# Optimization experiments

Measured on AMD Instinct MI355X. Metric: run time of the kernel, lower is better.

## Reference

```python
import jax, jax.numpy as jnp
import numpy as np
from jax import lax

V = 5          # IMU nodes
C = 128        # channels
T = 128        # timesteps
B = 128        # batch
K = 3          # st_kernel_size (non-causal)
V_TH = 0.8     # LIF threshold
TAU = 2.0      # LIF default tau (spikingjelly)
EPS = 1e-5


def setup_inputs() -> dict:
    key = jax.random.key(0)
    ks = jax.random.split(key, 6)
    # binary spike input [T, B, C, 2V]
    x_spike = (jax.random.uniform(ks[0], (T, B, C, 2 * V)) < 0.5).astype(jnp.float32)
    # modality fusion conv1d: [C, 2C, 1], kaiming-ish scale
    W_fusion = jax.random.normal(ks[1], (C, 2 * C, 1), jnp.float32) * (1.0 / np.sqrt(2 * C))
    gn1_w = jnp.ones((C,), jnp.float32)
    gn1_b = jnp.zeros((C,), jnp.float32)
    # node mixer conv1d over time: [V, V, K]
    W_mixer = jax.random.normal(ks[2], (V, V, K), jnp.float32) * (1.0 / np.sqrt(V * K))
    gn2_w = jnp.ones((V,), jnp.float32)
    gn2_b = jnp.zeros((V,), jnp.float32)
    # learnable adjacency: eye + 0.01*randn
    adj = jnp.eye(V, dtype=jnp.float32) + 0.01 * jax.random.normal(ks[3], (V, V), jnp.float32)
    return {"x_spike": x_spike, "W_fusion": W_fusion, "gn1_w": gn1_w, "gn1_b": gn1_b,
            "W_mixer": W_mixer, "gn2_w": gn2_w, "gn2_b": gn2_b, "adj": adj}


def groupnorm1(x, w, b):
    # single-group GroupNorm on [N, C, L]: normalize over (C, L) per sample
    mu = jnp.mean(x, axis=(1, 2), keepdims=True)
    var = jnp.var(x, axis=(1, 2), keepdims=True)
    xn = (x - mu) * lax.rsqrt(var + EPS)
    return xn * w[None, :, None] + b[None, :, None]


def lif_multistep(x_seq):
    # spikingjelly LIFNode, step_mode='m', decay_input=True, hard reset to 0
    def step(v, x):
        v = v + (x - v) / TAU
        s = (v >= V_TH).astype(x.dtype)
        v = v * (1.0 - s)
        return v, s
    _, spikes = lax.scan(step, jnp.zeros_like(x_seq[0]), x_seq)
    return spikes


def reference(x_spike, W_fusion, gn1_w, gn1_b, W_mixer, gn2_w, gn2_b, adj):
    Tn, Bn, Cn, N = x_spike.shape
    # ---- dual-modality fusion ----
    acc, gyr = x_spike[..., :V], x_spike[..., V:]
    fused = jnp.concatenate([acc, gyr], axis=2).reshape(Tn * Bn, 2 * Cn, V)  # [TB, 2C, V]
    y = jnp.einsum('oc,ncv->nov', W_fusion[:, :, 0], fused)                   # 1x1 conv
    y = groupnorm1(y, gn1_w, gn1_b)
    x_nodes = lif_multistep(y.reshape(Tn, Bn, Cn, V))                         # [T,B,C,V]
    # ---- adaptive topology temporal conv ----
    x_bt = x_nodes.transpose(1, 2, 3, 0).reshape(Bn * Cn, V, Tn)              # [BC, V, T]
    pad = K // 2
    x_bt = jnp.pad(x_bt, ((0, 0), (0, 0), (pad, pad)))
    sym = 0.5 * (adj + adj.T)
    masked_w = W_mixer * jax.nn.sigmoid(sym)[:, :, None]                      # [V, V, K]
    y_bt = lax.conv_general_dilated(x_bt, masked_w, (1,), 'VALID',
                                    dimension_numbers=('NCH', 'OIH', 'NCH'))
    y_bt = y_bt[..., :Tn]
    y_bt = groupnorm1(y_bt, gn2_w, gn2_b)
    y_mixed = y_bt.reshape(Bn, Cn, V, Tn).transpose(3, 0, 1, 2)               # [T,B,C,V]
    out = lif_multistep(y_mixed)
    return jnp.concatenate([out, out], axis=-1)                               # [T,B,C,2V]
```

## Files before the change

### kernel.cpp

```cpp
#include <hip/hip_runtime.h>
#include <cstdint>
#include <cstddef>

#define NV 5
#define NC 128
#define NT 128
#define NB 128
typedef unsigned long long ull;
typedef float f32x2 __attribute__((ext_vector_type(2)));
typedef float f32x4 __attribute__((ext_vector_type(4)));

__device__ __forceinline__ float fa(float a, float b){ return __fadd_rn(a,b); }
__device__ __forceinline__ float fm(float a, float b){ return __fmul_rn(a,b); }
__device__ __forceinline__ float fs(float a, float b){ return __fsub_rn(a,b); }

__device__ __forceinline__ f32x2 pkadd(f32x2 a, f32x2 b){
    f32x2 d; asm("v_pk_add_f32 %0, %1, %2" : "=v"(d) : "v"(a), "v"(b)); return d;
}
__device__ __forceinline__ f32x2 pkmul_lo(f32x2 a, f32x2 w){
    f32x2 d; asm("v_pk_mul_f32 %0, %1, %2 op_sel:[0,0] op_sel_hi:[1,0]"
                 : "=v"(d) : "v"(a), "v"(w)); return d;
}
__device__ __forceinline__ f32x2 pkmul_hi(f32x2 a, f32x2 w){
    f32x2 d; asm("v_pk_mul_f32 %0, %1, %2 op_sel:[0,1] op_sel_hi:[1,1]"
                 : "=v"(d) : "v"(a), "v"(w)); return d;
}

__device__ __forceinline__ float base80(const float* a)
{
    float r0=a[0],r1=a[1],r2=a[2],r3=a[3],r4=a[4],r5=a[5],r6=a[6],r7=a[7];
    #pragma unroll
    for (int i = 8; i < 80; i += 8) {
        r0=fa(r0,a[i+0]); r1=fa(r1,a[i+1]); r2=fa(r2,a[i+2]); r3=fa(r3,a[i+3]);
        r4=fa(r4,a[i+4]); r5=fa(r5,a[i+5]); r6=fa(r6,a[i+6]); r7=fa(r7,a[i+7]);
    }
    return fa(fa(fa(r0,r1),fa(r2,r3)), fa(fa(r4,r5),fa(r6,r7)));
}

__device__ __forceinline__ float base80v(const float* a, float mu)
{
    float r[8];
    #pragma unroll
    for (int j = 0; j < 8; ++j) { const float d = fs(a[j], mu); r[j] = fm(d, d); }
    #pragma unroll
    for (int i = 8; i < 80; i += 8)
        #pragma unroll
        for (int j = 0; j < 8; ++j) {
            const float d = fs(a[i + j], mu);
            r[j] = fa(r[j], fm(d, d));
        }
    return fa(fa(fa(r[0],r[1]),fa(r[2],r[3])), fa(fa(r[4],r[5]),fa(r[6],r[7])));
}

__global__ __launch_bounds__(256) void kT(const float* __restrict__ W,
                                          f32x4* __restrict__ Wt4)
{
    const int i = blockIdx.x * 256 + threadIdx.x;
    const int fcp = i >> 6, oL = i & 63;
    f32x4 p;
    p.x = W[oL * 256 + 2 * fcp];
    p.y = W[(oL + 64) * 256 + 2 * fcp];
    p.z = W[oL * 256 + 2 * fcp + 1];
    p.w = W[(oL + 64) * 256 + 2 * fcp + 1];
    Wt4[i] = p;
}

__global__ __launch_bounds__(256) void kA(const float* __restrict__ x,
                                          const f32x4* __restrict__ Wt4,
                                          const float* __restrict__ g1w,
                                          const float* __restrict__ g1b,
                                          float* __restrict__ y1)
{
    const int n0   = blockIdx.x * 8;
    const int tid  = threadIdx.x;
    const int lane = tid & 63;
    const int wv   = tid >> 6;

    __shared__ __align__(16) float xs[10240];

    {
        const float4* g0 = (const float4*)(x + (size_t)(n0 + 2 * wv) * 1280);
        const float4* g1 = g0 + 320;
        #pragma unroll
        for (int it = 0; it < 5; ++it) {
            const int k = it * 64 + lane;
            const float4 a = g0[k];
            const float4 b = g1[k];
            const float av[4] = {a.x, a.y, a.z, a.w};
            const float bv[4] = {b.x, b.y, b.z, b.w};
            int f = k * 4;
            #pragma unroll
            for (int e = 0; e < 4; ++e, ++f) {
                const int c  = f / 10;
                const int j  = f - c * 10;
                const int v  = (j < 5) ? j : j - 5;
                const int fc = (j < 5) ? c : c + 128;
                const int fcp = fc >> 1, sub = fc & 1;
                f32x2 pr; pr.x = av[e]; pr.y = bv[e];
                *(f32x2*)&xs[(fcp * 4 + wv) * 20 + sub * 10 + v * 2] = pr;
            }
        }
    }

    f32x2 accA[NV], accB[NV];
    #pragma unroll
    for (int v = 0; v < NV; ++v) { accA[v] = (f32x2){0.f,0.f}; accB[v] = (f32x2){0.f,0.f}; }

    const float* xw = xs + wv * 20;
    #pragma unroll 2
    for (int fcp = 0; fcp < 128; ++fcp) {
        const f32x4 wab = Wt4[fcp * 64 + lane];
        const float* row = xw + fcp * 80;
        const f32x4 Q0 = *(const f32x4*)&row[0];
        const f32x4 Q1 = *(const f32x4*)&row[4];
        const f32x4 Q2 = *(const f32x4*)&row[8];
        const f32x4 Q3 = *(const f32x4*)&row[12];
        const f32x4 Q4 = *(const f32x4*)&row[16];
        const f32x2 w01 = __builtin_shufflevector(wab, wab, 0, 1);
        const f32x2 w23 = __builtin_shufflevector(wab, wab, 2, 3);
        const f32x2 a0 = __builtin_shufflevector(Q0, Q0, 0, 1);
        const f32x2 a1 = __builtin_shufflevector(Q0, Q0, 2, 3);
        const f32x2 a2 = __builtin_shufflevector(Q1, Q1, 0, 1);
        const f32x2 a3 = __builtin_shufflevector(Q1, Q1, 2, 3);
        const f32x2 a4 = __builtin_shufflevector(Q2, Q2, 0, 1);
        const f32x2 b0 = __builtin_shufflevector(Q2, Q2, 2, 3);
        const f32x2 b1 = __builtin_shufflevector(Q3, Q3, 0, 1);
        const f32x2 b2 = __builtin_shufflevector(Q3, Q3, 2, 3);
        const f32x2 b3 = __builtin_shufflevector(Q4, Q4, 0, 1);
        const f32x2 b4 = __builtin_shufflevector(Q4, Q4, 2, 3);
        accA[0] = pkadd(accA[0], pkmul_lo(a0, w01));
        accA[1] = pkadd(accA[1], pkmul_lo(a1, w01));
        accA[2] = pkadd(accA[2], pkmul_lo(a2, w01));
        accA[3] = pkadd(accA[3], pkmul_lo(a3, w01));
        accA[4] = pkadd(accA[4], pkmul_lo(a4, w01));
        accB[0] = pkadd(accB[0], pkmul_hi(a0, w01));
        accB[1] = pkadd(accB[1], pkmul_hi(a1, w01));
        accB[2] = pkadd(accB[2], pkmul_hi(a2, w01));
        accB[3] = pkadd(accB[3], pkmul_hi(a3, w01));
        accB[4] = pkadd(accB[4], pkmul_hi(a4, w01));
        accA[0] = pkadd(accA[0], pkmul_lo(b0, w23));
        accA[1] = pkadd(accA[1], pkmul_lo(b1, w23));
        accA[2] = pkadd(accA[2], pkmul_lo(b2, w23));
        accA[3] = pkadd(accA[3], pkmul_lo(b3, w23));
        accA[4] = pkadd(accA[4], pkmul_lo(b4, w23));
        accB[0] = pkadd(accB[0], pkmul_hi(b0, w23));
        accB[1] = pkadd(accB[1], pkmul_hi(b1, w23));
        accB[2] = pkadd(accB[2], pkmul_hi(b2, w23));
        accB[3] = pkadd(accB[3], pkmul_hi(b3, w23));
        accB[4] = pkadd(accB[4], pkmul_hi(b4, w23));
    }
    __syncthreads();

    float* ys     = xs;
    float* statAf = xs + 5120;
    float* muS    = xs + 5152;
    float* rstdS  = xs + 5160;

    #pragma unroll
    for (int sl = 0; sl < 2; ++sl) {
        const int g = wv * 2 + sl;
        #pragma unroll
        for (int v = 0; v < NV; ++v) {
            ys[g * 640 + lane * 5 + v]        = sl ? accA[v].y : accA[v].x;
            ys[g * 640 + (lane + 64) * 5 + v] = sl ? accB[v].y : accB[v].x;
        }
    }
    __syncthreads();

    if (tid < 32) {
        const int g = tid >> 2, p = tid & 3;
        const float b0 = base80(&ys[g * 640 + (2 * p) * 80]);
        const float b1 = base80(&ys[g * 640 + (2 * p + 1) * 80]);
        statAf[g * 4 + p] = fa(b0, b1);
    }
    __syncthreads();
    if (tid < 8) {
        const int g = tid;
        const float* s = statAf + g * 4;
        const float tot = fa(fa(s[0], s[1]), fa(s[2], s[3]));
        muS[g] = __fdiv_rn(tot, 640.f);
    }
    __syncthreads();

    #pragma unroll
    for (int sl = 0; sl < 2; ++sl) {
        const int g = wv * 2 + sl;
        const float mu = muS[g];
        #pragma unroll
        for (int v = 0; v < NV; ++v) {
            const float aA = sl ? accA[v].y : accA[v].x;
            const float aB = sl ? accB[v].y : accB[v].x;
            const float dA = fs(aA, mu);
            const float dB = fs(aB, mu);
            ys[g * 640 + lane * 5 + v]        = fm(dA, dA);
            ys[g * 640 + (lane + 64) * 5 + v] = fm(dB, dB);
        }
    }
    __syncthreads();
    if (tid < 32) {
        const int g = tid >> 2, p = tid & 3;
        const float b0 = base80(&ys[g * 640 + (2 * p) * 80]);
        const float b1 = base80(&ys[g * 640 + (2 * p + 1) * 80]);
        statAf[g * 4 + p] = fa(b0, b1);
    }
    __syncthreads();
    if (tid < 8) {
        const int g = tid;
        const float* s = statAf + g * 4;
        const float tot = fa(fa(s[0], s[1]), fa(s[2], s[3]));
        const float var = __fdiv_rn(tot, 640.f);
        rstdS[g] = __fdiv_rn(1.f, __fsqrt_rn(fa(var, 1e-5f)));
    }
    __syncthreads();

    #pragma unroll
    for (int ch = 0; ch < 2; ++ch) {
        const int o = lane + ch * 64;
        const float wf = g1w[o], bf = g1b[o];
        #pragma unroll
        for (int sl = 0; sl < 2; ++sl) {
            const int g = wv * 2 + sl;
            const float mu = muS[g], rstd = rstdS[g];
            const int n = n0 + g;
            #pragma unroll
            for (int v = 0; v < NV; ++v) {
                const float av = ch ? (sl ? accB[v].y : accB[v].x)
                                    : (sl ? accA[v].y : accA[v].x);
                const float xn = fm(fs(av, mu), rstd);
                y1[(size_t)n * 640 + o * 5 + v] = fa(fm(xn, wf), bf);
            }
        }
    }
}

__global__ __launch_bounds__(320) void kB1(const float* __restrict__ y1,
                                           ulonglong2* __restrict__ masks)
{
    const int b   = blockIdx.x >> 1;
    const int c0  = (blockIdx.x & 1) * 64;
    const int tid = threadIdx.x;

    ull lo = 0ull, hi = 0ull;
    float vm = 0.f;
    const float* p = y1 + (size_t)b * 640 + (size_t)c0 * 5 + tid;
    for (int t0 = 0; t0 < NT; t0 += 16) {
        float xv[16];
        #pragma unroll
        for (int j = 0; j < 16; ++j)
            xv[j] = p[(size_t)(t0 + j) * (NB * 640)];
        #pragma unroll
        for (int j = 0; j < 16; ++j) {
            vm = fa(vm, fm(fs(xv[j], vm), 0.5f));
            if (vm >= 0.8f) {
                const int t = t0 + j;
                if (t < 64) lo |= 1ull << t; else hi |= 1ull << (t - 64);
                vm = 0.f;
            }
        }
    }
    masks[(size_t)b * 640 + (size_t)c0 * 5 + tid] = make_ulonglong2(lo, hi);
}

__device__ __forceinline__ float bitf(ull lo, ull hi, int t)
{
    if (t < 0 || t > 127) return 0.f;
    return (float)(((t < 64) ? (lo >> t) : (hi >> (t - 64))) & 1ull);
}

__global__ __launch_bounds__(512) void kB2(const ulonglong2* __restrict__ masks,
                                           const float* __restrict__ Wm,
                                           const float* __restrict__ g2w,
                                           const float* __restrict__ g2b,
                                           const float* __restrict__ adj,
                                           float* __restrict__ out)
{
    const int blk = blockIdx.x;
    const int b   = blk >> 5;
    const int c0  = (blk & 31) * 4;
    const int tid = threadIdx.x;
    const int p   = tid >> 7;
    const int lt  = tid & 127;

    __shared__ float mw_s[75];
    __shared__ ull   m_lo[4][5], m_hi[4][5];
    __shared__ float conv_s[4][5][128];
    __shared__ float spk_s[128][40];
    __shared__ float stat_s[4][8];
    __shared__ float mu_s[4], rstd_s[4];

    if (tid < 75) {
        const int oo = tid / 15, rem = tid % 15, ii = rem / 3;
        const float sym = fm(0.5f, fa(adj[oo * 5 + ii], adj[ii * 5 + oo]));
        const float e = (float)exp(-(double)sym);
        const float sig = __fdiv_rn(1.f, fa(1.f, e));
        mw_s[tid] = fm(Wm[tid], sig);
    }
    if (tid < 20) {
        const int pp = tid / 5, vv = tid % 5;
        const ulonglong2 m = masks[((size_t)b * 128 + c0 + pp) * 5 + vv];
        m_lo[pp][vv] = m.x; m_hi[pp][vv] = m.y;
    }
    __syncthreads();

    {
        float bv[5][3];
        #pragma unroll
        for (int i = 0; i < 5; ++i) {
            const ull lo = m_lo[p][i], hi = m_hi[p][i];
            #pragma unroll
            for (int k = 0; k < 3; ++k)
                bv[i][k] = bitf(lo, hi, lt - 1 + k);
        }
        #pragma unroll
        for (int o = 0; o < 5; ++o) {
            float res = 0.f;
            #pragma unroll
            for (int i = 0; i < 5; ++i)
                #pragma unroll
                for (int k = 0; k < 3; ++k)
                    res = fa(res, fm(mw_s[(o * 5 + i) * 3 + k], bv[i][k]));
            conv_s[p][o][lt] = res;
        }
    }
    __syncthreads();

    if (lt < 8)
        stat_s[p][lt] = base80(&conv_s[p][0][0] + lt * 80);
    __syncthreads();
    if (lt == 0) {
        const float* s = stat_s[p];
        const float tot = fa(fa(fa(s[0],s[1]),fa(s[2],s[3])),
                             fa(fa(s[4],s[5]),fa(s[6],s[7])));
        mu_s[p] = __fdiv_rn(tot, 640.f);
    }
    __syncthreads();

    if (lt < 8)
        stat_s[p][lt] = base80v(&conv_s[p][0][0] + lt * 80, mu_s[p]);
    __syncthreads();
    if (lt == 0) {
        const float* s = stat_s[p];
        const float tot = fa(fa(fa(s[0],s[1]),fa(s[2],s[3])),
                             fa(fa(s[4],s[5]),fa(s[6],s[7])));
        const float var = __fdiv_rn(tot, 640.f);
        rstd_s[p] = __fdiv_rn(1.f, __fsqrt_rn(fa(var, 1e-5f)));
    }
    __syncthreads();

    if (lt < 5) {
        const int o = lt;
        const float mu = mu_s[p], rstd = rstd_s[p];
        const float gw = g2w[o], gb = g2b[o];
        float vm = 0.f;
        for (int t = 0; t < NT; ++t) {
            const float z  = conv_s[p][o][t];
            const float xn = fm(fs(z, mu), rstd);
            const float yn = fa(fm(xn, gw), gb);
            vm = fa(vm, fm(fs(yn, vm), 0.5f));
            const bool sp = (vm >= 0.8f);
            if (sp) vm = 0.f;
            const float so = sp ? 1.f : 0.f;
            spk_s[t][p * 10 + o]     = so;
            spk_s[t][p * 10 + 5 + o] = so;
        }
    }
    __syncthreads();

    for (int q = tid; q < 1280; q += 512) {
        const int t = q / 10, s = q - t * 10;
        float4* dst = (float4*)(out + ((size_t)(t * NB + b) * 1280 + c0 * 10));
        dst[s] = reinterpret_cast<const float4*>(&spk_s[t][0])[s];
    }
}

extern "C" void kernel_launch(void* const* d_in, const int* in_sizes, int n_in,
                              void* d_out, int out_size, void* d_ws, size_t ws_size,
                              hipStream_t stream)
{
    const float* x   = (const float*)d_in[0];
    const float* W   = (const float*)d_in[1];
    const float* g1w = (const float*)d_in[2];
    const float* g1b = (const float*)d_in[3];
    const float* Wm  = (const float*)d_in[4];
    const float* g2w = (const float*)d_in[5];
    const float* g2b = (const float*)d_in[6];
    const float* adj = (const float*)d_in[7];
    float* out = (float*)d_out;

    float* y1 = (float*)d_ws;
    ulonglong2* masks = (ulonglong2*)((char*)d_ws + (64u << 20));
    f32x4* Wt4 = (f32x4*)((char*)d_ws + (80u << 20));

    hipLaunchKernelGGL(kT, dim3(32), dim3(256), 0, stream, W, Wt4);
    hipLaunchKernelGGL(kA, dim3(NT * NB / 8), dim3(256), 0, stream,
                       x, Wt4, g1w, g1b, y1);
    hipLaunchKernelGGL(kB1, dim3(NB * 2), dim3(320), 0, stream,
                       y1, masks);
    hipLaunchKernelGGL(kB2, dim3(4096), dim3(512), 0, stream,
                       masks, Wm, g2w, g2b, adj, out);
}
```

Before: 179.6 us.

## Encode binary spike input as wave ballot bitmasks and feed packed MACs from SGPRs

New measurement: 417.7 us. 2.33x slower.

```diff
diff --git a/kernel.cpp b/kernel.cpp
--- a/kernel.cpp
+++ b/kernel.cpp
@@ -7,6 +7,7 @@
 #define NT 128
 #define NB 128
 typedef unsigned long long ull;
+typedef unsigned int u32;
 typedef float f32x2 __attribute__((ext_vector_type(2)));
 typedef float f32x4 __attribute__((ext_vector_type(4)));
 
@@ -17,13 +18,13 @@
 __device__ __forceinline__ f32x2 pkadd(f32x2 a, f32x2 b){
     f32x2 d; asm("v_pk_add_f32 %0, %1, %2" : "=v"(d) : "v"(a), "v"(b)); return d;
 }
-__device__ __forceinline__ f32x2 pkmul_lo(f32x2 a, f32x2 w){
+__device__ __forceinline__ f32x2 pkmul_lo_s(f32x2 xs_, f32x2 w){
     f32x2 d; asm("v_pk_mul_f32 %0, %1, %2 op_sel:[0,0] op_sel_hi:[1,0]"
-                 : "=v"(d) : "v"(a), "v"(w)); return d;
-}
-__device__ __forceinline__ f32x2 pkmul_hi(f32x2 a, f32x2 w){
+                 : "=v"(d) : "s"(xs_), "v"(w)); return d;
+}
+__device__ __forceinline__ f32x2 pkmul_hi_s(f32x2 xs_, f32x2 w){
     f32x2 d; asm("v_pk_mul_f32 %0, %1, %2 op_sel:[0,1] op_sel_hi:[1,1]"
-                 : "=v"(d) : "v"(a), "v"(w)); return d;
+                 : "=v"(d) : "s"(xs_), "v"(w)); return d;
 }
 
 __device__ __forceinline__ float base80(const float* a)
@@ -76,85 +77,59 @@
     const int lane = tid & 63;
     const int wv   = tid >> 6;
 
-    __shared__ __align__(16) float xs[10240];
-
-    {
-        const float4* g0 = (const float4*)(x + (size_t)(n0 + 2 * wv) * 1280);
-        const float4* g1 = g0 + 320;
-        #pragma unroll
-        for (int it = 0; it < 5; ++it) {
-            const int k = it * 64 + lane;
-            const float4 a = g0[k];
-            const float4 b = g1[k];
-            const float av[4] = {a.x, a.y, a.z, a.w};
-            const float bv[4] = {b.x, b.y, b.z, b.w};
-            int f = k * 4;
-            #pragma unroll
-            for (int e = 0; e < 4; ++e, ++f) {
-                const int c  = f / 10;
-                const int j  = f - c * 10;
-                const int v  = (j < 5) ? j : j - 5;
-                const int fc = (j < 5) ? c : c + 128;
-                const int fcp = fc >> 1, sub = fc & 1;
-                f32x2 pr; pr.x = av[e]; pr.y = bv[e];
-                *(f32x2*)&xs[(fcp * 4 + wv) * 20 + sub * 10 + v * 2] = pr;
+    __shared__ float ys[8 * 640 + 48];
+
+    f32x2 accA[NV], accB[NV];
+    #pragma unroll
+    for (int v = 0; v < NV; ++v) { accA[v] = (f32x2){0.f,0.f}; accB[v] = (f32x2){0.f,0.f}; }
+
+    #pragma unroll
+    for (int ph = 0; ph < 2; ++ph) {
+        ull msk[2][NV][2];
+        #pragma unroll
+        for (int smp = 0; smp < 2; ++smp) {
+            const float* xb = x + (size_t)(n0 + 2 * wv + smp) * 1280 + ph * 5;
+            #pragma unroll
+            for (int v = 0; v < NV; ++v)
+                #pragma unroll
+                for (int w = 0; w < 2; ++w) {
+                    const float xv = xb[(w * 64 + lane) * 10 + v];
+                    msk[smp][v][w] = __ballot(xv != 0.0f);
+                }
+        }
+
+        #pragma unroll 2
+        for (int fcp2 = 0; fcp2 < 64; ++fcp2) {
+            const int fcl  = 2 * fcp2;
+            const int word = fcl >> 6;
+            const int b    = fcl & 63;
+            const f32x4 wab = Wt4[(ph * 64 + fcp2) * 64 + lane];
+            const f32x2 w01 = __builtin_shufflevector(wab, wab, 0, 1);
+            const f32x2 w23 = __builtin_shufflevector(wab, wab, 2, 3);
+            #pragma unroll
+            for (int v = 0; v < NV; ++v) {
+                const u32 c0 = (u32)(msk[0][v][word] >> b) & 3u;
+                const u32 c1 = (u32)(msk[1][v][word] >> b) & 3u;
+                const u32 l0 = (c0 & 1u)  * 0x3F800000u;
+                const u32 h0 = (c1 & 1u)  * 0x3F800000u;
+                const u32 l1 = (c0 >> 1)  * 0x3F800000u;
+                const u32 h1 = (c1 >> 1)  * 0x3F800000u;
+                const ull p0 = (ull)l0 | ((ull)h0 << 32);
+                const ull p1 = (ull)l1 | ((ull)h1 << 32);
+                f32x2 xp0, xp1;
+                __builtin_memcpy(&xp0, &p0, 8);
+                __builtin_memcpy(&xp1, &p1, 8);
+                accA[v] = pkadd(accA[v], pkmul_lo_s(xp0, w01));
+                accB[v] = pkadd(accB[v], pkmul_hi_s(xp0, w01));
+                accA[v] = pkadd(accA[v], pkmul_lo_s(xp1, w23));
+                accB[v] = pkadd(accB[v], pkmul_hi_s(xp1, w23));
             }
         }
     }
 
-    f32x2 accA[NV], accB[NV];
-    #pragma unroll
-    for (int v = 0; v < NV; ++v) { accA[v] = (f32x2){0.f,0.f}; accB[v] = (f32x2){0.f,0.f}; }
-
-    const float* xw = xs + wv * 20;
-    #pragma unroll 2
-    for (int fcp = 0; fcp < 128; ++fcp) {
-        const f32x4 wab = Wt4[fcp * 64 + lane];
-        const float* row = xw + fcp * 80;
-        const f32x4 Q0 = *(const f32x4*)&row[0];
-        const f32x4 Q1 = *(const f32x4*)&row[4];
-        const f32x4 Q2 = *(const f32x4*)&row[8];
-        const f32x4 Q3 = *(const f32x4*)&row[12];
-        const f32x4 Q4 = *(const f32x4*)&row[16];
-        const f32x2 w01 = __builtin_shufflevector(wab, wab, 0, 1);
-        const f32x2 w23 = __builtin_shufflevector(wab, wab, 2, 3);
-        const f32x2 a0 = __builtin_shufflevector(Q0, Q0, 0, 1);
-        const f32x2 a1 = __builtin_shufflevector(Q0, Q0, 2, 3);
-        const f32x2 a2 = __builtin_shufflevector(Q1, Q1, 0, 1);
-        const f32x2 a3 = __builtin_shufflevector(Q1, Q1, 2, 3);
-        const f32x2 a4 = __builtin_shufflevector(Q2, Q2, 0, 1);
-        const f32x2 b0 = __builtin_shufflevector(Q2, Q2, 2, 3);
-        const f32x2 b1 = __builtin_shufflevector(Q3, Q3, 0, 1);
-        const f32x2 b2 = __builtin_shufflevector(Q3, Q3, 2, 3);
-        const f32x2 b3 = __builtin_shufflevector(Q4, Q4, 0, 1);
-        const f32x2 b4 = __builtin_shufflevector(Q4, Q4, 2, 3);
-        accA[0] = pkadd(accA[0], pkmul_lo(a0, w01));
-        accA[1] = pkadd(accA[1], pkmul_lo(a1, w01));
-        accA[2] = pkadd(accA[2], pkmul_lo(a2, w01));
-        accA[3] = pkadd(accA[3], pkmul_lo(a3, w01));
-        accA[4] = pkadd(accA[4], pkmul_lo(a4, w01));
-        accB[0] = pkadd(accB[0], pkmul_hi(a0, w01));
-        accB[1] = pkadd(accB[1], pkmul_hi(a1, w01));
-        accB[2] = pkadd(accB[2], pkmul_hi(a2, w01));
-        accB[3] = pkadd(accB[3], pkmul_hi(a3, w01));
-        accB[4] = pkadd(accB[4], pkmul_hi(a4, w01));
-        accA[0] = pkadd(accA[0], pkmul_lo(b0, w23));
-        accA[1] = pkadd(accA[1], pkmul_lo(b1, w23));
-        accA[2] = pkadd(accA[2], pkmul_lo(b2, w23));
-        accA[3] = pkadd(accA[3], pkmul_lo(b3, w23));
-        accA[4] = pkadd(accA[4], pkmul_lo(b4, w23));
-        accB[0] = pkadd(accB[0], pkmul_hi(b0, w23));
-        accB[1] = pkadd(accB[1], pkmul_hi(b1, w23));
-        accB[2] = pkadd(accB[2], pkmul_hi(b2, w23));
-        accB[3] = pkadd(accB[3], pkmul_hi(b3, w23));
-        accB[4] = pkadd(accB[4], pkmul_hi(b4, w23));
-    }
-    __syncthreads();
-
-    float* ys     = xs;
-    float* statAf = xs + 5120;
-    float* muS    = xs + 5152;
-    float* rstdS  = xs + 5160;
+    float* statAf = ys + 5120;
+    float* muS    = ys + 5152;
+    float* rstdS  = ys + 5160;
 
     #pragma unroll
     for (int sl = 0; sl < 2; ++sl) {
```
